# Kernel optimization log

Measured on AMD Instinct MI355X. Metric: run time of the kernel, lower is better.

The kernel has to match this reference:

```python
import jax, jax.numpy as jnp
import numpy as np

NEG_POS_RATIO = 3
BETA = 1.0
ALPHA = 2.0


def _smooth_ex_loss(pred, tgt):
    # a = beta / (1 - exp(-alpha)); c = a - beta - beta/alpha
    a = BETA / (1.0 - np.exp(-ALPHA))
    c = a - BETA - BETA / ALPHA
    diff = jnp.abs(pred - tgt)
    return jnp.where(diff < 1.0,
                     a * (diff + (jnp.exp(-ALPHA * diff) - 1.0) / ALPHA),
                     BETA * diff + c)


def setup_inputs() -> dict:
    key = jax.random.key(0)
    k1, k2, k3, k4 = jax.random.split(key, 4)
    B, P, C = 128, 8732, 21
    return {
        "confidence": jax.random.normal(k1, (B, P, C), dtype=jnp.float32),
        "predicted_locations": jax.random.normal(k2, (B, P, 4), dtype=jnp.float32),
        "labels": jax.random.randint(k3, (B, P), 0, C, dtype=jnp.int64),
        "gt_locations": jax.random.normal(k4, (B, P, 4), dtype=jnp.float32),
    }


def reference(confidence, predicted_locations, labels, gt_locations):
    # confidence: [B, P, C]; labels: [B, P]; locations: [B, P, 4]
    logp = jax.nn.log_softmax(confidence, axis=2)
    pos_mask = labels > 0

    # --- hard negative mining (no-grad in original) ---
    bg_loss = jax.lax.stop_gradient(-logp[:, :, 0])          # [B, P]
    num_pos = pos_mask.sum(axis=1, keepdims=True)             # [B, 1]
    num_neg = num_pos * NEG_POS_RATIO
    mined = jnp.where(pos_mask, -jnp.inf, bg_loss)
    idx = jnp.argsort(-mined, axis=1)                         # descending sort
    orders = jnp.argsort(idx, axis=1)                         # rank of each prior
    neg_mask = orders < num_neg
    mask = pos_mask | neg_mask                                # [B, P]

    # --- classification loss: sum of CE over mined priors ---
    per_elem_ce = -jnp.take_along_axis(logp, labels[..., None], axis=2)[..., 0]
    classification_loss = jnp.sum(jnp.where(mask, per_elem_ce, 0.0))

    # --- localization loss: smooth-ex loss over positive priors ---
    loc = _smooth_ex_loss(predicted_locations, gt_locations)  # [B, P, 4]
    smooth_sum = jnp.sum(jnp.where(pos_mask[..., None], loc, 0.0))

    n_pos_total = pos_mask.sum().astype(jnp.float32)
    return (smooth_sum / n_pos_total, classification_loss / n_pos_total)
```

## Files before the change

kernel.cpp:

```cpp
#include <hip/hip_runtime.h>
#include <cstdint>


#define B_ 128
#define P_ 8732
#define C_ 21
constexpr int BPR = 16;
constexpr int TPB = 256;
constexpr int GRID = B_ * BPR;
constexpr int STRIDE = BPR * TPB;

typedef float f32x4u __attribute__((ext_vector_type(4), aligned(4)));

__device__ __forceinline__ float waveSumF(float v) {
#pragma unroll
  for (int o = 32; o; o >>= 1) v += __shfl_down(v, o);
  return v;
}
__device__ __forceinline__ int waveSumI(int v) {
#pragma unroll
  for (int o = 32; o; o >>= 1) v += __shfl_down(v, o);
  return v;
}
__device__ __forceinline__ double waveSumD(double v) {
#pragma unroll
  for (int o = 32; o; o >>= 1) v += __shfl_down(v, o);
  return v;
}

__global__ __launch_bounds__(TPB) void k_main(
    const float* __restrict__ conf, const float* __restrict__ pred,
    const int* __restrict__ labels, const float* __restrict__ gt,
    float4* __restrict__ part) {
  const int tid = threadIdx.x;
  const int row = blockIdx.x >> 4;
  const int sub = blockIdx.x & 15;
  const int t0 = sub * TPB + tid;
  const size_t rowBase = (size_t)row * P_;
  const float4* pred4 = (const float4*)pred;
  const float4* gt4 = (const float4*)gt;

  float sm = 0.f, cp = 0.f, cn = 0.f;
  int np = 0;

  for (int p = t0; p < P_; p += STRIDE) {
    const size_t gp = rowBase + p;
    const float* r = conf + gp * C_;
    float f[C_];
    {
      const f32x4u* r4 = (const f32x4u*)r;
      const f32x4u v0 = r4[0], v1 = r4[1], v2 = r4[2], v3 = r4[3], v4 = r4[4];
      f[0] = v0.x; f[1] = v0.y; f[2] = v0.z; f[3] = v0.w;
      f[4] = v1.x; f[5] = v1.y; f[6] = v1.z; f[7] = v1.w;
      f[8] = v2.x; f[9] = v2.y; f[10] = v2.z; f[11] = v2.w;
      f[12] = v3.x; f[13] = v3.y; f[14] = v3.z; f[15] = v3.w;
      f[16] = v4.x; f[17] = v4.y; f[18] = v4.z; f[19] = v4.w;
      f[20] = r[20];
    }
    const int lab = labels[gp];
    const float4 pr = pred4[gp];
    const float4 gv = gt4[gp];

    float m = f[0];
#pragma unroll
    for (int c = 1; c < C_; ++c) m = fmaxf(m, f[c]);
    float s = 0.f;
    float xl = f[0];
#pragma unroll
    for (int c = 0; c < C_; ++c) {
      s += __expf(f[c] - m);
      if (c > 0) xl = (lab == c) ? f[c] : xl;
    }
    const float ce = m + __logf(s) - xl;

    if (lab > 0) {
      np++;
      cp += ce;
      const float A = 1.1565176427496657f;
      const float Cc = -0.3434823572503343f;
      float d;
      d = fabsf(pr.x - gv.x); sm += (d < 1.f) ? A * (d + (__expf(-2.f * d) - 1.f) * 0.5f) : d + Cc;
      d = fabsf(pr.y - gv.y); sm += (d < 1.f) ? A * (d + (__expf(-2.f * d) - 1.f) * 0.5f) : d + Cc;
      d = fabsf(pr.z - gv.z); sm += (d < 1.f) ? A * (d + (__expf(-2.f * d) - 1.f) * 0.5f) : d + Cc;
      d = fabsf(pr.w - gv.w); sm += (d < 1.f) ? A * (d + (__expf(-2.f * d) - 1.f) * 0.5f) : d + Cc;
    } else {
      cn += ce;
    }
  }

  float a0 = waveSumF(sm), a1 = waveSumF(cp), a2 = waveSumF(cn);
  int a3 = waveSumI(np);
  __shared__ float s0[4], s1[4], s2[4];
  __shared__ int s3[4];
  const int wid = tid >> 6, lane = tid & 63;
  if (lane == 0) { s0[wid] = a0; s1[wid] = a1; s2[wid] = a2; s3[wid] = a3; }
  __syncthreads();
  if (tid == 0) {
    part[blockIdx.x] = make_float4(
        s0[0] + s0[1] + s0[2] + s0[3], s1[0] + s1[1] + s1[2] + s1[3],
        s2[0] + s2[1] + s2[2] + s2[3], (float)(s3[0] + s3[1] + s3[2] + s3[3]));
  }
}

__device__ __forceinline__ unsigned keyCE(const float* __restrict__ conf,
                                          const int* __restrict__ labels,
                                          int b, int p, float& ce) {
  const float* row = conf + ((size_t)b * P_ + p) * C_;
  float m = row[0];
  for (int c = 1; c < C_; ++c) m = fmaxf(m, row[c]);
  float s = 0.f;
  for (int c = 0; c < C_; ++c) s += __expf(row[c] - m);
  const float lse = m + __logf(s);
  const int lab = labels[(size_t)b * P_ + p];
  ce = lse - row[lab];
  if (lab > 0) return 0u;
  unsigned u = __float_as_uint(lse - row[0]);
  u = (u & 0x80000000u) ? ~u : (u | 0x80000000u);
  return u ? u : 1u;
}

__global__ __launch_bounds__(128) void k_tail(
    const float4* __restrict__ part, const float* __restrict__ conf,
    const int* __restrict__ labels, float* __restrict__ out) {
  const int tid = threadIdx.x;
  const int wid = tid >> 6, lane = tid & 63;
  __shared__ int s_np[B_], s_flag[B_];
  __shared__ double sdA[2], sdB[2], sdC[2];
  __shared__ int siN[2];
  __shared__ double s_extra;
  __shared__ int icnt[2];
  __shared__ float fsum[2];

  double sm = 0.0, cp = 0.0, cnSel = 0.0;
  int npr = 0;
  {
    double cn = 0.0;
#pragma unroll
    for (int i = 0; i < BPR; ++i) {
      const float4 v = part[tid * BPR + i];
      sm += (double)v.x;
      cp += (double)v.y;
      cn += (double)v.z;
      npr += (int)v.w;
    }
    s_np[tid] = npr;
    const int fl = (3 * npr < P_ - npr) ? 1 : 0;
    s_flag[tid] = fl;
    if (!fl) cnSel = cn;
  }
  const double t1 = waveSumD(sm), t2 = waveSumD(cp), t3 = waveSumD(cnSel);
  const int t4 = waveSumI(npr);
  if (lane == 0) { sdA[wid] = t1; sdB[wid] = t2; sdC[wid] = t3; siN[wid] = t4; }
  if (tid == 0) s_extra = 0.0;
  __syncthreads();

  for (int b = 0; b < B_; ++b) {
    if (!s_flag[b]) continue;
    const int need = 3 * s_np[b];
    unsigned long long lo = 1, hi = 0xFFFFFFFFull, ans = 1;
    while (lo <= hi) {
      const unsigned long long mid = lo + ((hi - lo) >> 1);
      int c = 0;
      float dummy;
      for (int p = tid; p < P_; p += 128)
        if ((unsigned long long)keyCE(conf, labels, b, p, dummy) >= mid) c++;
      c = waveSumI(c);
      if (lane == 0) icnt[wid] = c;
      __syncthreads();
      const int tot = icnt[0] + icnt[1];
      if (tot >= need) { ans = mid; lo = mid + 1; } else { hi = mid - 1; }
      __syncthreads();
    }
    int cgt = 0;
    float sgt = 0.f;
    for (int p = tid; p < P_; p += 128) {
      float ce;
      const unsigned long long k = keyCE(conf, labels, b, p, ce);
      if (k > ans) { cgt++; sgt += ce; }
    }
    cgt = waveSumI(cgt);
    sgt = waveSumF(sgt);
    if (lane == 0) { icnt[wid] = cgt; fsum[wid] = sgt; }
    __syncthreads();
    if (tid == 0) {
      const int gtot = icnt[0] + icnt[1];
      double s = (double)(fsum[0] + fsum[1]);
      int rm = need - gtot;
      int taken = 0;
      for (int p = 0; p < P_ && taken < rm; ++p) {
        float ce;
        if (keyCE(conf, labels, b, p, ce) == ans) { s += ce; taken++; }
      }
      s_extra += s;
    }
    __syncthreads();
  }

  if (tid == 0) {
    const double G0 = sdA[0] + sdA[1];
    const double G1 = sdB[0] + sdB[1];
    const double G2 = sdC[0] + sdC[1] + s_extra;
    const double N = (double)(siN[0] + siN[1]);
    out[0] = (float)(G0 / N);
    out[1] = (float)((G1 + G2) / N);
  }
}

extern "C" void kernel_launch(void* const* d_in, const int* in_sizes, int n_in,
                              void* d_out, int out_size, void* d_ws, size_t ws_size,
                              hipStream_t stream) {
  const float* conf = (const float*)d_in[0];
  const float* pred = (const float*)d_in[1];
  const int* labels = (const int*)d_in[2];
  const float* gt = (const float*)d_in[3];
  float* out = (float*)d_out;

  float4* part = (float4*)d_ws;

  hipLaunchKernelGGL(k_main, dim3(GRID), dim3(TPB), 0, stream,
                     conf, pred, labels, gt, part);
  hipLaunchKernelGGL(k_tail, dim3(1), dim3(128), 0, stream,
                     part, conf, labels, out);
}
```

Measured before the change: 39.75 us.

## Stage confidence rows into LDS via async global_load_lds double buffering

The main kernel now has each wave own a contiguous span of 312 priors. It streams 64-prior chunks of the confidence tensor into LDS with global_load_lds, double-buffered, and prefetches the labels and locations for the next chunk while computing the current one. This replaces the strided, unaligned per-thread 84-byte row loads with coalesced 16-byte transfers, meant to improve memory efficiency on this bandwidth-bound pass. In exchange it adds LDS usage, a smaller 128-thread block, explicit vmcnt waits, and branchless masked accumulation.

```diff
diff --git a/kernel.cpp b/kernel.cpp
--- a/kernel.cpp
+++ b/kernel.cpp
@@ -5,12 +5,16 @@
 #define B_ 128
 #define P_ 8732
 #define C_ 21
-constexpr int BPR = 16;
-constexpr int TPB = 256;
-constexpr int GRID = B_ * BPR;
-constexpr int STRIDE = BPR * TPB;
-
-typedef float f32x4u __attribute__((ext_vector_type(4), aligned(4)));
+constexpr int TPB = 128;
+constexpr int SPR = 28;
+constexpr int SPAN = 312;
+constexpr int NCHK = 5;
+constexpr int GRID = B_ * SPR / 2;
+constexpr int SLOTS = SPR / 2;
+constexpr int CHB = 64 * C_ * 4;
+
+typedef const __attribute__((address_space(1))) uint32_t* gas_u32p;
+typedef __attribute__((address_space(3))) uint32_t* las_u32p;
 
 __device__ __forceinline__ float waveSumF(float v) {
 #pragma unroll
@@ -28,77 +32,131 @@
   return v;
 }
 
-__global__ __launch_bounds__(TPB) void k_main(
+__device__ __forceinline__ void stage(const char* g, float* l, int bytes, int lane) {
+#pragma unroll
+  for (int j = 0; j < 6; ++j) {
+    const int off = (j << 10) + (lane << 4);
+    if (off < bytes)
+      __builtin_amdgcn_global_load_lds((gas_u32p)(g + off),
+                                       (las_u32p)(l + (j << 8)), 16, 0, 0);
+  }
+}
+
+#define SMEX(d) (((d) < 1.f) ? (1.1565176427496657f * ((d) + (__expf(-2.f * (d)) - 1.f) * 0.5f)) \
+                             : ((d) - 0.3434823572503343f))
+
+__device__ __forceinline__ void prior21(const float* lp, int lab, float4 pr, float4 gv,
+                                        bool act, float& sm, float& cp, float& cn, int& np) {
+  const float f0 = lp[0], f1 = lp[1], f2 = lp[2], f3 = lp[3], f4 = lp[4];
+  const float f5 = lp[5], f6 = lp[6], f7 = lp[7], f8 = lp[8], f9 = lp[9];
+  const float f10 = lp[10], f11 = lp[11], f12 = lp[12], f13 = lp[13], f14 = lp[14];
+  const float f15 = lp[15], f16 = lp[16], f17 = lp[17], f18 = lp[18], f19 = lp[19];
+  const float f20 = lp[20];
+  float m = fmaxf(fmaxf(fmaxf(fmaxf(f0, f1), fmaxf(f2, f3)),
+                        fmaxf(fmaxf(f4, f5), fmaxf(f6, f7))),
+                  fmaxf(fmaxf(fmaxf(f8, f9), fmaxf(f10, f11)),
+                        fmaxf(fmaxf(f12, f13), fmaxf(f14, f15))));
+  m = fmaxf(m, fmaxf(fmaxf(fmaxf(f16, f17), fmaxf(f18, f19)), f20));
+  float s = __expf(f0 - m) + __expf(f1 - m) + __expf(f2 - m) + __expf(f3 - m);
+  s += __expf(f4 - m) + __expf(f5 - m) + __expf(f6 - m) + __expf(f7 - m);
+  s += __expf(f8 - m) + __expf(f9 - m) + __expf(f10 - m) + __expf(f11 - m);
+  s += __expf(f12 - m) + __expf(f13 - m) + __expf(f14 - m) + __expf(f15 - m);
+  s += __expf(f16 - m) + __expf(f17 - m) + __expf(f18 - m) + __expf(f19 - m);
+  s += __expf(f20 - m);
+  float xl = f0;
+  xl = (lab == 1) ? f1 : xl;   xl = (lab == 2) ? f2 : xl;
+  xl = (lab == 3) ? f3 : xl;   xl = (lab == 4) ? f4 : xl;
+  xl = (lab == 5) ? f5 : xl;   xl = (lab == 6) ? f6 : xl;
+  xl = (lab == 7) ? f7 : xl;   xl = (lab == 8) ? f8 : xl;
+  xl = (lab == 9) ? f9 : xl;   xl = (lab == 10) ? f10 : xl;
+  xl = (lab == 11) ? f11 : xl; xl = (lab == 12) ? f12 : xl;
+  xl = (lab == 13) ? f13 : xl; xl = (lab == 14) ? f14 : xl;
+  xl = (lab == 15) ? f15 : xl; xl = (lab == 16) ? f16 : xl;
+  xl = (lab == 17) ? f17 : xl; xl = (lab == 18) ? f18 : xl;
+  xl = (lab == 19) ? f19 : xl; xl = (lab == 20) ? f20 : xl;
+  const float ce = m + __logf(s) - xl;
+
+  float d, smx;
+  d = fabsf(pr.x - gv.x); smx = SMEX(d);
+  d = fabsf(pr.y - gv.y); smx += SMEX(d);
+  d = fabsf(pr.z - gv.z); smx += SMEX(d);
+  d = fabsf(pr.w - gv.w); smx += SMEX(d);
+
+  const bool pos = act && (lab > 0);
+  sm += pos ? smx : 0.f;
+  cp += pos ? ce : 0.f;
+  cn += (act && lab == 0) ? ce : 0.f;
+  np += pos ? 1 : 0;
+}
+
+__global__ __launch_bounds__(TPB, 3) void k_main(
     const float* __restrict__ conf, const float* __restrict__ pred,
     const int* __restrict__ labels, const float* __restrict__ gt,
     float4* __restrict__ part) {
+  __shared__ __align__(16) float sbuf[2][2][64 * C_];
+  __shared__ float redf[6];
+  __shared__ int redi[2];
   const int tid = threadIdx.x;
-  const int row = blockIdx.x >> 4;
-  const int sub = blockIdx.x & 15;
-  const int t0 = sub * TPB + tid;
-  const size_t rowBase = (size_t)row * P_;
+  const int wid = tid >> 6, lane = tid & 63;
+  const int row = blockIdx.x / SLOTS;
+  const int pair = blockIdx.x % SLOTS;
+  const int s = pair * 2 + wid;
+  const int ps = s * SPAN;
+  const int spc = min(SPAN, P_ - ps);
+  const size_t rp = (size_t)row * P_;
+  const char* cbase = (const char*)conf + (rp + (size_t)ps) * (C_ * 4);
   const float4* pred4 = (const float4*)pred;
   const float4* gt4 = (const float4*)gt;
+  float* wbuf0 = sbuf[wid][0];
+  float* wbuf1 = sbuf[wid][1];
+
+  stage(cbase, wbuf0, 64 * C_ * 4, lane);
+  int labr;
+  float4 prr, gvr;
+  {
+    const size_t gp = rp + ps + lane;
+    labr = labels[gp];
+    prr = pred4[gp];
+    gvr = gt4[gp];
+  }
+  asm volatile("s_waitcnt vmcnt(0)" ::: "memory");
+  __builtin_amdgcn_sched_barrier(0);
 
   float sm = 0.f, cp = 0.f, cn = 0.f;
   int np = 0;
 
-  for (int p = t0; p < P_; p += STRIDE) {
-    const size_t gp = rowBase + p;
-    const float* r = conf + gp * C_;
-    float f[C_];
-    {
-      const f32x4u* r4 = (const f32x4u*)r;
-      const f32x4u v0 = r4[0], v1 = r4[1], v2 = r4[2], v3 = r4[3], v4 = r4[4];
-      f[0] = v0.x; f[1] = v0.y; f[2] = v0.z; f[3] = v0.w;
-      f[4] = v1.x; f[5] = v1.y; f[6] = v1.z; f[7] = v1.w;
-      f[8] = v2.x; f[9] = v2.y; f[10] = v2.z; f[11] = v2.w;
-      f[12] = v3.x; f[13] = v3.y; f[14] = v3.z; f[15] = v3.w;
-      f[16] = v4.x; f[17] = v4.y; f[18] = v4.z; f[19] = v4.w;
-      f[20] = r[20];
-    }
-    const int lab = labels[gp];
-    const float4 pr = pred4[gp];
-    const float4 gv = gt4[gp];
-
-    float m = f[0];
-#pragma unroll
-    for (int c = 1; c < C_; ++c) m = fmaxf(m, f[c]);
-    float s = 0.f;
-    float xl = f[0];
-#pragma unroll
-    for (int c = 0; c < C_; ++c) {
-      s += __expf(f[c] - m);
-      if (c > 0) xl = (lab == c) ? f[c] : xl;
-    }
-    const float ce = m + __logf(s) - xl;
-
-    if (lab > 0) {
-      np++;
-      cp += ce;
-      const float A = 1.1565176427496657f;
-      const float Cc = -0.3434823572503343f;
-      float d;
-      d = fabsf(pr.x - gv.x); sm += (d < 1.f) ? A * (d + (__expf(-2.f * d) - 1.f) * 0.5f) : d + Cc;
-      d = fabsf(pr.y - gv.y); sm += (d < 1.f) ? A * (d + (__expf(-2.f * d) - 1.f) * 0.5f) : d + Cc;
-      d = fabsf(pr.z - gv.z); sm += (d < 1.f) ? A * (d + (__expf(-2.f * d) - 1.f) * 0.5f) : d + Cc;
-      d = fabsf(pr.w - gv.w); sm += (d < 1.f) ? A * (d + (__expf(-2.f * d) - 1.f) * 0.5f) : d + Cc;
-    } else {
-      cn += ce;
-    }
-  }
-
-  float a0 = waveSumF(sm), a1 = waveSumF(cp), a2 = waveSumF(cn);
-  int a3 = waveSumI(np);
-  __shared__ float s0[4], s1[4], s2[4];
-  __shared__ int s3[4];
-  const int wid = tid >> 6, lane = tid & 63;
-  if (lane == 0) { s0[wid] = a0; s1[wid] = a1; s2[wid] = a2; s3[wid] = a3; }
+#pragma unroll
+  for (int k = 0; k < NCHK; ++k) {
+    float* cbuf = (k & 1) ? wbuf1 : wbuf0;
+    float* nbuf = (k & 1) ? wbuf0 : wbuf1;
+    int labn = 0;
+    float4 prn = make_float4(0, 0, 0, 0), gvn = prn;
+    if (k + 1 < NCHK) {
+      const int cntn = min(64, spc - ((k + 1) << 6));
+      stage(cbase + (size_t)(k + 1) * CHB, nbuf, cntn * (C_ * 4), lane);
+      int idx = ((k + 1) << 6) + lane;
+      if (idx >= spc) idx = spc - 1;
+      const size_t gp = rp + ps + idx;
+      labn = labels[gp];
+      prn = pred4[gp];
+      gvn = gt4[gp];
+    }
+
+    const int cnt = min(64, spc - (k << 6));
+    prior21(&cbuf[lane * C_], labr, prr, gvr, lane < cnt, sm, cp, cn, np);
+
+    asm volatile("s_waitcnt vmcnt(0)" ::: "memory");
+    __builtin_amdgcn_sched_barrier(0);
+    labr = labn; prr = prn; gvr = gvn;
+  }
+
+  const float r0 = waveSumF(sm), r1 = waveSumF(cp), r2 = waveSumF(cn);
+  const int r3 = waveSumI(np);
+  if (lane == 0) { redf[wid] = r0; redf[2 + wid] = r1; redf[4 + wid] = r2; redi[wid] = r3; }
   __syncthreads();
   if (tid == 0) {
-    part[blockIdx.x] = make_float4(
-        s0[0] + s0[1] + s0[2] + s0[3], s1[0] + s1[1] + s1[2] + s1[3],
-        s2[0] + s2[1] + s2[2] + s2[3], (float)(s3[0] + s3[1] + s3[2] + s3[3]));
+    part[blockIdx.x] = make_float4(redf[0] + redf[1], redf[2] + redf[3],
+                                   redf[4] + redf[5], (float)(redi[0] + redi[1]));
   }
 }
 
@@ -136,8 +194,8 @@
   {
     double cn = 0.0;
 #pragma unroll
-    for (int i = 0; i < BPR; ++i) {
-      const float4 v = part[tid * BPR + i];
+    for (int i = 0; i < SLOTS; ++i) {
+      const float4 v = part[tid * SLOTS + i];
       sm += (double)v.x;
       cp += (double)v.y;
       cn += (double)v.z;
@@ -184,14 +242,14 @@
     __syncthreads();
     if (tid == 0) {
       const int gtot = icnt[0] + icnt[1];
-      double s = (double)(fsum[0] + fsum[1]);
+      double sx = (double)(fsum[0] + fsum[1]);
       int rm = need - gtot;
       int taken = 0;
       for (int p = 0; p < P_ && taken < rm; ++p) {
         float ce;
-        if (keyCE(conf, labels, b, p, ce) == ans) { s += ce; taken++; }
+        if (keyCE(conf, labels, b, p, ce) == ans) { sx += ce; taken++; }
       }
-      s_extra += s;
+      s_extra += sx;
     }
     __syncthreads();
   }
```

Result: slower. 41.98 us (+5.6%).
